# Optimization experiments

Hardware: AMD Instinct MI355X
Metric: run time of the kernel (lower is better)

## Reference

```python
import jax, jax.numpy as jnp
import numpy as np

N = 50000
E = 800000
F_IN = 128
H1, C1 = 8, 32   # conv1: heads=8, out_channels=32 -> concat 256
H2, C2 = 1, 32   # conv2: heads=1, out_channels=32
NEG_SLOPE = 0.2


def setup_inputs() -> dict:
    key = jax.random.key(0)
    ks = jax.random.split(key, 10)
    x = jax.random.normal(ks[0], (N, F_IN), dtype=jnp.float32)
    edge_index = jax.random.randint(ks[1], (2, E), 0, N, dtype=jnp.int64)
    s1 = 1.0 / np.sqrt(F_IN)
    s2 = 1.0 / np.sqrt(H1 * C1)
    return {
        "x": x,
        "edge_index": edge_index,
        "W1": jax.random.normal(ks[2], (F_IN, H1 * C1), dtype=jnp.float32) * s1,
        "b1": jnp.zeros((H1 * C1,), dtype=jnp.float32),
        "att_src1": jax.random.normal(ks[3], (1, H1, C1), dtype=jnp.float32) * s1,
        "att_dst1": jax.random.normal(ks[4], (1, H1, C1), dtype=jnp.float32) * s1,
        "W2": jax.random.normal(ks[5], (H1 * C1, H2 * C2), dtype=jnp.float32) * s2,
        "b2": jnp.zeros((H2 * C2,), dtype=jnp.float32),
        "att_src2": jax.random.normal(ks[6], (1, H2, C2), dtype=jnp.float32) * s2,
        "att_dst2": jax.random.normal(ks[7], (1, H2, C2), dtype=jnp.float32) * s2,
    }


def _gat_conv(x, src, tgt, W, b, att_src, att_dst, heads, ch):
    n = x.shape[0]
    h = (x @ W).reshape(n, heads, ch)                      # [N,H,C]
    a_s = jnp.sum(h * att_src, axis=-1)                    # [N,H]
    a_d = jnp.sum(h * att_dst, axis=-1)                    # [N,H]
    e = jax.nn.leaky_relu(a_s[src] + a_d[tgt], NEG_SLOPE)  # [E',H]
    m = jax.ops.segment_max(e, tgt, num_segments=n)        # per-target max
    e = jnp.exp(e - m[tgt])
    denom = jax.ops.segment_sum(e, tgt, num_segments=n)
    alpha = e / denom[tgt]                                 # edge softmax over in-edges
    msg = h[src] * alpha[:, :, None]                       # [E',H,C]
    out = jax.ops.segment_sum(msg, tgt, num_segments=n)    # scatter-add at targets
    return out.reshape(n, heads * ch) + b


def reference(x, edge_index, W1, b1, att_src1, att_dst1, W2, b2, att_src2, att_dst2):
    n = x.shape[0]
    # PyG GATConv adds self-loops inside each conv; same augmented edge set both layers.
    loops = jnp.arange(n, dtype=edge_index.dtype)
    src = jnp.concatenate([edge_index[0], loops])  # message source j
    tgt = jnp.concatenate([edge_index[1], loops])  # message target i
    h = _gat_conv(x, src, tgt, W1, b1, att_src1, att_dst1, H1, C1)
    h = jax.nn.elu(h)
    h = _gat_conv(h, src, tgt, W2, b2, att_src2, att_dst2, H2, C2)
    return jax.nn.elu(h)
```

## Files before the change

kernel.cpp:

```cpp
#include <hip/hip_runtime.h>
#include <hip/hip_fp16.h>
#include <cmath>

#define NNODES 50000
#define NEDGES 800000
#define ETOT   (NEDGES + NNODES)
#define FIN    128
#define NH1    8
#define NC1    32
#define HC1    256
#define NC2    32

#define NBUCK  ((NNODES + 63) / 64)
#define BCAP   1536
#define EPB    4096

using half8 = __attribute__((ext_vector_type(8))) _Float16;
using f32x4 = __attribute__((ext_vector_type(4))) float;

__device__ __forceinline__ float lrelu(float x) { return x > 0.f ? x : 0.2f * x; }

#define NB_W1    ((FIN * HC1 + 255) / 256)
#define NB_W2    ((HC1 * NC2 + 255) / 256)
#define NB_P1    ((ETOT + EPB - 1) / EPB)

__global__ void __launch_bounds__(256) prep_k(const float* __restrict__ W1,
        __half* __restrict__ W1t, const float* __restrict__ W2, __half* __restrict__ W2t,
        const int* __restrict__ ei, int* __restrict__ bcnt, unsigned* __restrict__ pairs) {
    __shared__ int lcnt[NBUCK];
    __shared__ int gbase[NBUCK];
    int b = blockIdx.x;
    if (b < NB_W1) {
        int i = b * 256 + threadIdx.x;
        if (i < FIN * HC1) {
            int k = i / HC1, n = i - k * HC1;
            W1t[(size_t)n * FIN + k] = __float2half(W1[i]);
        }
        return;
    }
    b -= NB_W1;
    if (b < NB_W2) {
        int i = b * 256 + threadIdx.x;
        if (i < HC1 * NC2) {
            int k = i / NC2, n = i - k * NC2;
            W2t[(size_t)n * HC1 + k] = __float2half(W2[i]);
        }
        return;
    }
    b -= NB_W2;
    for (int i = threadIdx.x; i < NBUCK; i += 256) lcnt[i] = 0;
    __syncthreads();
    int e0 = b * EPB + threadIdx.x;
    int bk[16]; int rk[16]; unsigned pk[16];
#pragma unroll
    for (int k = 0; k < 16; ++k) {
        int e = e0 + k * 256;
        bk[k] = -1;
        if (e < ETOT) {
            int s, t;
            if (e < NEDGES) { s = ei[e]; t = ei[NEDGES + e]; } else { s = t = e - NEDGES; }
            int bb = t >> 6;
            bk[k] = bb;
            rk[k] = atomicAdd(&lcnt[bb], 1);
            pk[k] = ((unsigned)(t & 63) << 16) | (unsigned)s;
        }
    }
    __syncthreads();
    for (int i = threadIdx.x; i < NBUCK; i += 256) {
        int c = lcnt[i];
        gbase[i] = c ? atomicAdd(bcnt + i, c) : 0;
    }
    __syncthreads();
#pragma unroll
    for (int k = 0; k < 16; ++k) {
        if (bk[k] >= 0) {
            int pos = gbase[bk[k]] + rk[k];
            if (pos < BCAP) pairs[(size_t)bk[k] * BCAP + pos] = pk[k];
        }
    }
}

__global__ void __launch_bounds__(256) combo_k(const unsigned* __restrict__ pairs,
        const int* __restrict__ bcnt, int* __restrict__ csr,
        int* __restrict__ rp_start, int* __restrict__ cntT,
        const float* __restrict__ x, const __half* __restrict__ Bt,
        const float* __restrict__ att_s, const float* __restrict__ att_d,
        __half* __restrict__ C, float* __restrict__ as_, float* __restrict__ ad_) {
    __shared__ int lcnt64[64];
    __shared__ int base64[64];
    __shared__ unsigned short binned[BCAP];
    if (blockIdx.x < NBUCK) {
        int b = blockIdx.x;
        int nb = bcnt[b]; nb = nb < BCAP ? nb : BCAP;
        if (threadIdx.x < 64) lcnt64[threadIdx.x] = 0;
        __syncthreads();
        unsigned ps[6]; int rks[6]; bool vld[6];
#pragma unroll
        for (int k = 0; k < 6; ++k) {
            int i = threadIdx.x + k * 256;
            vld[k] = i < nb;
            if (vld[k]) {
                unsigned p = pairs[(size_t)b * BCAP + i];
                ps[k] = p;
                rks[k] = atomicAdd(&lcnt64[p >> 16], 1);
            }
        }
        __syncthreads();
        if (threadIdx.x < 64) {
            int v = lcnt64[threadIdx.x];
            int inc = v;
#pragma unroll
            for (int ofs = 1; ofs < 64; ofs <<= 1) {
                int o = __shfl_up(inc, ofs, 64);
                if ((int)threadIdx.x >= ofs) inc += o;
            }
            base64[threadIdx.x] = inc - v;
        }
        __syncthreads();
#pragma unroll
        for (int k = 0; k < 6; ++k) {
            if (vld[k]) binned[base64[ps[k] >> 16] + rks[k]] = (unsigned short)(ps[k] & 0xFFFFu);
        }
        __syncthreads();
        for (int i = threadIdx.x; i < nb; i += 256)
            csr[(size_t)b * BCAP + i] = binned[i];
        if (threadIdx.x < 64) {
            int t = b * 64 + threadIdx.x;
            if (t < NNODES) {
                rp_start[t] = b * BCAP + base64[threadIdx.x];
                cntT[t] = lcnt64[threadIdx.x];
            }
        }
        return;
    }
    const _Float16* Bf = (const _Float16*)Bt;
    int blk = blockIdx.x - NBUCK;
    int wv = threadIdx.x >> 6, lane = threadIdx.x & 63;
    int r16 = lane & 15, kg = lane >> 4;
    int bm = blk * 16;
    int arow = bm + r16; if (arow >= NNODES) arow = NNODES - 1;
    f32x4 acc[4] = {};
#pragma unroll
    for (int kt = 0; kt < FIN; kt += 32) {
        const float4* xr = (const float4*)(x + (size_t)arow * FIN + kt + kg * 8);
        float4 f0 = xr[0], f1 = xr[1];
        half8 a;
        a[0] = (_Float16)f0.x; a[1] = (_Float16)f0.y; a[2] = (_Float16)f0.z; a[3] = (_Float16)f0.w;
        a[4] = (_Float16)f1.x; a[5] = (_Float16)f1.y; a[6] = (_Float16)f1.z; a[7] = (_Float16)f1.w;
#pragma unroll
        for (int ct = 0; ct < 4; ++ct) {
            int col = wv * 64 + ct * 16 + r16;
            half8 bfr = *(const half8*)(Bf + (size_t)col * FIN + kt + kg * 8);
            acc[ct] = __builtin_amdgcn_mfma_f32_16x16x32_f16(a, bfr, acc[ct], 0, 0, 0);
        }
    }
#pragma unroll
    for (int ct = 0; ct < 4; ++ct)
#pragma unroll
        for (int r = 0; r < 4; ++r) {
            int orow = bm + kg * 4 + r;
            if (orow < NNODES)
                C[(size_t)orow * HC1 + wv * 64 + ct * 16 + r16] = __float2half(acc[ct][r]);
        }
#pragma unroll
    for (int P = 0; P < 2; ++P) {
        int head = 2 * wv + P;
        float ws0 = att_s[head * 32 + r16], ws1 = att_s[head * 32 + 16 + r16];
        float wd0 = att_d[head * 32 + r16], wd1 = att_d[head * 32 + 16 + r16];
        float sv[4], dv[4];
#pragma unroll
        for (int r = 0; r < 4; ++r) {
            sv[r] = acc[2 * P][r] * ws0 + acc[2 * P + 1][r] * ws1;
            dv[r] = acc[2 * P][r] * wd0 + acc[2 * P + 1][r] * wd1;
#pragma unroll
            for (int ofs = 1; ofs < 16; ofs <<= 1) {
                sv[r] += __shfl_xor(sv[r], ofs, 64);
                dv[r] += __shfl_xor(dv[r], ofs, 64);
            }
        }
#pragma unroll
        for (int r = 0; r < 4; ++r) {
            int orow = bm + kg * 4 + r;
            if (r16 == r && orow < NNODES) {
                as_[orow * NH1 + head] = sv[r];
                ad_[orow * NH1 + head] = dv[r];
            }
        }
    }
}

__global__ void __launch_bounds__(256) mgemm2_k(const __half* __restrict__ A,
        const __half* __restrict__ Bt, const float* __restrict__ att_s,
        const float* __restrict__ att_d, __half* __restrict__ C,
        float* __restrict__ as_, float* __restrict__ ad_) {
    const _Float16* Af = (const _Float16*)A;
    const _Float16* Bf = (const _Float16*)Bt;
    int wv = threadIdx.x >> 6, lane = threadIdx.x & 63;
    int r16 = lane & 15, kg = lane >> 4;
    int bm = blockIdx.x * 64 + wv * 16;
    int arow = bm + r16; if (arow >= NNODES) arow = NNODES - 1;
    f32x4 acc[2] = {};
#pragma unroll
    for (int kt = 0; kt < HC1; kt += 32) {
        half8 a = *(const half8*)(Af + (size_t)arow * HC1 + kt + kg * 8);
#pragma unroll
        for (int ct = 0; ct < 2; ++ct) {
            half8 b = *(const half8*)(Bf + (size_t)(ct * 16 + r16) * HC1 + kt + kg * 8);
            acc[ct] = __builtin_amdgcn_mfma_f32_16x16x32_f16(a, b, acc[ct], 0, 0, 0);
        }
    }
#pragma unroll
    for (int ct = 0; ct < 2; ++ct)
#pragma unroll
        for (int r = 0; r < 4; ++r) {
            int orow = bm + kg * 4 + r;
            if (orow < NNODES)
                C[(size_t)orow * NC2 + ct * 16 + r16] = __float2half(acc[ct][r]);
        }
    float ws0 = att_s[r16], ws1 = att_s[16 + r16];
    float wd0 = att_d[r16], wd1 = att_d[16 + r16];
    float sv[4], dv[4];
#pragma unroll
    for (int r = 0; r < 4; ++r) {
        sv[r] = acc[0][r] * ws0 + acc[1][r] * ws1;
        dv[r] = acc[0][r] * wd0 + acc[1][r] * wd1;
#pragma unroll
        for (int ofs = 1; ofs < 16; ofs <<= 1) {
            sv[r] += __shfl_xor(sv[r], ofs, 64);
            dv[r] += __shfl_xor(dv[r], ofs, 64);
        }
    }
#pragma unroll
    for (int r = 0; r < 4; ++r) {
        int orow = bm + kg * 4 + r;
        if (r16 == r && orow < NNODES) { as_[orow] = sv[r]; ad_[orow] = dv[r]; }
    }
}

__global__ void __launch_bounds__(256) gather1_k(const int* __restrict__ rp_start,
        const int* __restrict__ cntT, const int* __restrict__ csr,
        const __half* __restrict__ h, const float* __restrict__ as_,
        const float* __restrict__ ad_, const float* __restrict__ bias,
        __half* __restrict__ out) {
    int t = blockIdx.x * 4 + (threadIdx.x >> 6);
    int lane = threadIdx.x & 63;
    if (t >= NNODES) return;
    int hh = lane & 7;
    int hd = lane >> 3;
    float adv = ad_[t * NH1 + hh];
    int n = cntT[t];
    const int* cb = csr + rp_start[t];
    const uint2* h4 = (const uint2*)h;
    float4 acc = make_float4(0.f, 0.f, 0.f, 0.f);
    float dpart = 0.f;

    int slot = lane >> 3;
    bool val0 = slot < n;
    int sj0 = cb[val0 ? slot : 0];
    float a0 = as_[sj0 * NH1 + hh];

    for (int i = 0; i < n; i += 8) {
        int ii = i + 8 + slot;
        bool val1 = ii < n;
        int sj1 = cb[val1 ? ii : 0];
        float a1 = as_[sj1 * NH1 + hh];
        float p = val0 ? expf(lrelu(a0 + adv)) : 0.f;
        dpart += p;
        uint2 raw[8];
#pragma unroll
        for (int j = 0; j < 8; ++j) {
            int s = __shfl(sj0, 8 * j, 64);
            raw[j] = h4[(size_t)s * 64 + lane];
        }
#pragma unroll
        for (int j = 0; j < 8; ++j) {
            float al = __shfl(p, 8 * j + hd, 64);
            float2 f0 = __half22float2(*(const __half2*)&raw[j].x);
            float2 f1 = __half22float2(*(const __half2*)&raw[j].y);
            acc.x += al * f0.x; acc.y += al * f0.y;
            acc.z += al * f1.x; acc.w += al * f1.y;
        }
        sj0 = sj1; a0 = a1; val0 = val1;
    }
    dpart += __shfl_xor(dpart, 8, 64);
    dpart += __shfl_xor(dpart, 16, 64);
    dpart += __shfl_xor(dpart, 32, 64);
    float inv = __shfl(1.f / dpart, hd, 64);
    float4 bv = ((const float4*)bias)[lane];
    float4 r;
    r.x = acc.x * inv + bv.x; r.y = acc.y * inv + bv.y;
    r.z = acc.z * inv + bv.z; r.w = acc.w * inv + bv.w;
    r.x = r.x > 0.f ? r.x : expm1f(r.x);
    r.y = r.y > 0.f ? r.y : expm1f(r.y);
    r.z = r.z > 0.f ? r.z : expm1f(r.z);
    r.w = r.w > 0.f ? r.w : expm1f(r.w);
    __half2 p0 = __floats2half2_rn(r.x, r.y);
    __half2 p1 = __floats2half2_rn(r.z, r.w);
    uint2 w; w.x = *(unsigned*)&p0; w.y = *(unsigned*)&p1;
    ((uint2*)out)[(size_t)t * 64 + lane] = w;
}

__global__ void __launch_bounds__(256) gather2_k(const int* __restrict__ rp_start,
        const int* __restrict__ cntT, const int* __restrict__ csr,
        const __half* __restrict__ h, const float* __restrict__ as_,
        const float* __restrict__ ad_, const float* __restrict__ bias,
        float* __restrict__ out) {
    int t = blockIdx.x * 4 + (threadIdx.x >> 6);
    int lane = threadIdx.x & 63;
    if (t >= NNODES) return;
    int q = lane >> 3, f = lane & 7;
    float adv = ad_[t];
    int n = cntT[t];
    const int* cb = csr + rp_start[t];
    const uint2* h8 = (const uint2*)h;
    float4 acc = make_float4(0.f, 0.f, 0.f, 0.f);
    float dpart = 0.f;

    bool val0 = q < n;
    int sj0 = cb[val0 ? q : 0];
    float a0 = as_[sj0];

    for (int i = 0; i < n; i += 8) {
        int ii = i + 8 + q;
        bool val1 = ii < n;
        int sj1 = cb[val1 ? ii : 0];
        float a1 = as_[sj1];
        float p = val0 ? expf(lrelu(a0 + adv)) : 0.f;
        dpart += p;
        uint2 raw[8];
#pragma unroll
        for (int j = 0; j < 8; ++j) {
            int sj = __shfl(sj0, 8 * j, 64);
            raw[j] = h8[(size_t)sj * 8 + f];
        }
#pragma unroll
        for (int j = 0; j < 8; ++j) {
            float al = __shfl(p, 8 * j, 64);
            float2 f0 = __half22float2(*(const __half2*)&raw[j].x);
            float2 f1 = __half22float2(*(const __half2*)&raw[j].y);
            acc.x += al * f0.x; acc.y += al * f0.y;
            acc.z += al * f1.x; acc.w += al * f1.y;
        }
        sj0 = sj1; a0 = a1; val0 = val1;
    }
    dpart += __shfl_xor(dpart, 8, 64);
    dpart += __shfl_xor(dpart, 16, 64);
    dpart += __shfl_xor(dpart, 32, 64);
    if (q == 0) {
        float inv = 1.f / dpart;
        float4 bv = ((const float4*)bias)[f];
        float4 r;
        r.x = acc.x * inv + bv.x; r.y = acc.y * inv + bv.y;
        r.z = acc.z * inv + bv.z; r.w = acc.w * inv + bv.w;
        r.x = r.x > 0.f ? r.x : expm1f(r.x);
        r.y = r.y > 0.f ? r.y : expm1f(r.y);
        r.z = r.z > 0.f ? r.z : expm1f(r.z);
        r.w = r.w > 0.f ? r.w : expm1f(r.w);
        ((float4*)out)[(size_t)t * 8 + f] = r;
    }
}

extern "C" void kernel_launch(void* const* d_in, const int* in_sizes, int n_in,
                              void* d_out, int out_size, void* d_ws, size_t ws_size,
                              hipStream_t stream) {
    const float* x    = (const float*)d_in[0];
    const int*   ei   = (const int*)d_in[1];
    const float* W1   = (const float*)d_in[2];
    const float* b1   = (const float*)d_in[3];
    const float* as1w = (const float*)d_in[4];
    const float* ad1w = (const float*)d_in[5];
    const float* W2   = (const float*)d_in[6];
    const float* b2   = (const float*)d_in[7];
    const float* as2w = (const float*)d_in[8];
    const float* ad2w = (const float*)d_in[9];
    float* out = (float*)d_out;

    float* ws = (float*)d_ws;
    size_t off = 0;
    __half* h1h  = (__half*)(ws + off); off += (size_t)NNODES * HC1 / 2;
    __half* out1h= (__half*)(ws + off); off += (size_t)NNODES * HC1 / 2;
    __half* h2h  = (__half*)(ws + off); off += (size_t)NNODES * NC2 / 2;
    __half* W1t  = (__half*)(ws + off); off += (size_t)FIN * HC1 / 2;
    __half* W2t  = (__half*)(ws + off); off += (size_t)HC1 * NC2 / 2;
    float* as1  = ws + off; off += (size_t)NNODES * NH1;
    float* ad1  = ws + off; off += (size_t)NNODES * NH1;
    float* as2  = ws + off; off += NNODES;
    float* ad2  = ws + off; off += NNODES;
    unsigned* pairs = (unsigned*)(ws + off); off += (size_t)NBUCK * BCAP;
    int* csr      = (int*)(ws + off); off += (size_t)NBUCK * BCAP;
    int* bcnt     = (int*)(ws + off); off += NBUCK;
    int* rp_start = (int*)(ws + off); off += NNODES;
    int* cntT     = (int*)(ws + off); off += NNODES;

    hipMemsetAsync(bcnt, 0, (size_t)NBUCK * 4, stream);
    prep_k<<<NB_W1 + NB_W2 + NB_P1, 256, 0, stream>>>(W1, W1t, W2, W2t, ei, bcnt, pairs);
    combo_k<<<NBUCK + (NNODES + 15) / 16, 256, 0, stream>>>(
        pairs, bcnt, csr, rp_start, cntT, x, W1t, as1w, ad1w, h1h, as1, ad1);

    gather1_k<<<(NNODES + 3) / 4, 256, 0, stream>>>(rp_start, cntT, csr, h1h, as1, ad1, b1, out1h);

    mgemm2_k<<<(NNODES + 63) / 64, 256, 0, stream>>>(out1h, W2t, as2w, ad2w, h2h, as2, ad2);
    gather2_k<<<(NNODES + 3) / 4, 256, 0, stream>>>(rp_start, cntT, csr, h2h, as2, ad2, b2, out);
}
```

Baseline: 198.2 us.

## Fuse layer-2 GEMM into gather1 and move layer-1 GEMM into prep kernel

The layer-2 projection (256->32) and its attention logits are now computed inside gather1 straight from the per-node output held in shared memory. This removes the out1h round trip through global memory and drops the separate mgemm2 kernel. The layer-1 MFMA GEMM moves into the first kernel alongside edge bucketing and reads W1 directly as strided fp32 instead of a pre-transposed fp16 copy, so it no longer waits on the CSR finalisation. The trade-offs are uncoalesced scalar W1 loads in the GEMM and a scalar per-wave dot product in gather1 in place of MFMA.

```diff
diff --git a/kernel.cpp b/kernel.cpp
--- a/kernel.cpp
+++ b/kernel.cpp
@@ -20,220 +20,167 @@
 
 __device__ __forceinline__ float lrelu(float x) { return x > 0.f ? x : 0.2f * x; }
 
-#define NB_W1    ((FIN * HC1 + 255) / 256)
-#define NB_W2    ((HC1 * NC2 + 255) / 256)
-#define NB_P1    ((ETOT + EPB - 1) / EPB)
-
-__global__ void __launch_bounds__(256) prep_k(const float* __restrict__ W1,
-        __half* __restrict__ W1t, const float* __restrict__ W2, __half* __restrict__ W2t,
+#define NB_MG1 ((NNODES + 15) / 16)
+#define NB_P1  ((ETOT + EPB - 1) / EPB)
+#define NB_W2  ((HC1 * NC2 + 255) / 256)
+
+__global__ void __launch_bounds__(256) fused1_k(const float* __restrict__ x,
+        const float* __restrict__ W1, const float* __restrict__ att_s,
+        const float* __restrict__ att_d, __half* __restrict__ C,
+        float* __restrict__ as_, float* __restrict__ ad_,
+        const float* __restrict__ W2, __half* __restrict__ W2t,
         const int* __restrict__ ei, int* __restrict__ bcnt, unsigned* __restrict__ pairs) {
     __shared__ int lcnt[NBUCK];
     __shared__ int gbase[NBUCK];
     int b = blockIdx.x;
-    if (b < NB_W1) {
-        int i = b * 256 + threadIdx.x;
-        if (i < FIN * HC1) {
-            int k = i / HC1, n = i - k * HC1;
-            W1t[(size_t)n * FIN + k] = __float2half(W1[i]);
+    if (b < NB_MG1) {
+        int wv = threadIdx.x >> 6, lane = threadIdx.x & 63;
+        int r16 = lane & 15, kg = lane >> 4;
+        int bm = b * 16;
+        int arow = bm + r16; if (arow >= NNODES) arow = NNODES - 1;
+        f32x4 acc[4] = {};
+#pragma unroll
+        for (int kt = 0; kt < FIN; kt += 32) {
+            const float4* xr = (const float4*)(x + (size_t)arow * FIN + kt + kg * 8);
+            float4 f0 = xr[0], f1 = xr[1];
+            half8 a;
+            a[0] = (_Float16)f0.x; a[1] = (_Float16)f0.y; a[2] = (_Float16)f0.z; a[3] = (_Float16)f0.w;
+            a[4] = (_Float16)f1.x; a[5] = (_Float16)f1.y; a[6] = (_Float16)f1.z; a[7] = (_Float16)f1.w;
+#pragma unroll
+            for (int ct = 0; ct < 4; ++ct) {
+                int col = wv * 64 + ct * 16 + r16;
+                half8 bf;
+#pragma unroll
+                for (int j = 0; j < 8; ++j)
+                    bf[j] = (_Float16)W1[(size_t)(kt + kg * 8 + j) * HC1 + col];
+                acc[ct] = __builtin_amdgcn_mfma_f32_16x16x32_f16(a, bf, acc[ct], 0, 0, 0);
+            }
+        }
+#pragma unroll
+        for (int ct = 0; ct < 4; ++ct)
+#pragma unroll
+            for (int r = 0; r < 4; ++r) {
+                int orow = bm + kg * 4 + r;
+                if (orow < NNODES)
+                    C[(size_t)orow * HC1 + wv * 64 + ct * 16 + r16] = __float2half(acc[ct][r]);
+            }
+#pragma unroll
+        for (int P = 0; P < 2; ++P) {
+            int head = 2 * wv + P;
+            float ws0 = att_s[head * 32 + r16], ws1 = att_s[head * 32 + 16 + r16];
+            float wd0 = att_d[head * 32 + r16], wd1 = att_d[head * 32 + 16 + r16];
+            float sv[4], dv[4];
+#pragma unroll
+            for (int r = 0; r < 4; ++r) {
+                sv[r] = acc[2 * P][r] * ws0 + acc[2 * P + 1][r] * ws1;
+                dv[r] = acc[2 * P][r] * wd0 + acc[2 * P + 1][r] * wd1;
+#pragma unroll
+                for (int ofs = 1; ofs < 16; ofs <<= 1) {
+                    sv[r] += __shfl_xor(sv[r], ofs, 64);
+                    dv[r] += __shfl_xor(dv[r], ofs, 64);
+                }
+            }
+#pragma unroll
+            for (int r = 0; r < 4; ++r) {
+                int orow = bm + kg * 4 + r;
+                if (r16 == r && orow < NNODES) {
+                    as_[orow * NH1 + head] = sv[r];
+                    ad_[orow * NH1 + head] = dv[r];
+                }
+            }
         }
         return;
     }
-    b -= NB_W1;
-    if (b < NB_W2) {
+    b -= NB_MG1;
+    if (b < NB_P1) {
+        for (int i = threadIdx.x; i < NBUCK; i += 256) lcnt[i] = 0;
+        __syncthreads();
+        int e0 = b * EPB + threadIdx.x;
+        int bk[16]; int rk[16]; unsigned pk[16];
+#pragma unroll
+        for (int k = 0; k < 16; ++k) {
+            int e = e0 + k * 256;
+            bk[k] = -1;
+            if (e < ETOT) {
+                int s, t;
+                if (e < NEDGES) { s = ei[e]; t = ei[NEDGES + e]; } else { s = t = e - NEDGES; }
+                int bb = t >> 6;
+                bk[k] = bb;
+                rk[k] = atomicAdd(&lcnt[bb], 1);
+                pk[k] = ((unsigned)(t & 63) << 16) | (unsigned)s;
+            }
+        }
+        __syncthreads();
+        for (int i = threadIdx.x; i < NBUCK; i += 256) {
+            int c = lcnt[i];
+            gbase[i] = c ? atomicAdd(bcnt + i, c) : 0;
+        }
+        __syncthreads();
+#pragma unroll
+        for (int k = 0; k < 16; ++k) {
+            if (bk[k] >= 0) {
+                int pos = gbase[bk[k]] + rk[k];
+                if (pos < BCAP) pairs[(size_t)bk[k] * BCAP + pos] = pk[k];
+            }
+        }
+        return;
+    }
+    b -= NB_P1;
+    {
         int i = b * 256 + threadIdx.x;
         if (i < HC1 * NC2) {
             int k = i / NC2, n = i - k * NC2;
             W2t[(size_t)n * HC1 + k] = __float2half(W2[i]);
         }
-        return;
-    }
-    b -= NB_W2;
-    for (int i = threadIdx.x; i < NBUCK; i += 256) lcnt[i] = 0;
-    __syncthreads();
-    int e0 = b * EPB + threadIdx.x;
-    int bk[16]; int rk[16]; unsigned pk[16];
-#pragma unroll
-    for (int k = 0; k < 16; ++k) {
-        int e = e0 + k * 256;
-        bk[k] = -1;
-        if (e < ETOT) {
-            int s, t;
-            if (e < NEDGES) { s = ei[e]; t = ei[NEDGES + e]; } else { s = t = e - NEDGES; }
-            int bb = t >> 6;
-            bk[k] = bb;
-            rk[k] = atomicAdd(&lcnt[bb], 1);
-            pk[k] = ((unsigned)(t & 63) << 16) | (unsigned)s;
-        }
-    }
-    __syncthreads();
-    for (int i = threadIdx.x; i < NBUCK; i += 256) {
-        int c = lcnt[i];
-        gbase[i] = c ? atomicAdd(bcnt + i, c) : 0;
-    }
-    __syncthreads();
-#pragma unroll
-    for (int k = 0; k < 16; ++k) {
-        if (bk[k] >= 0) {
-            int pos = gbase[bk[k]] + rk[k];
-            if (pos < BCAP) pairs[(size_t)bk[k] * BCAP + pos] = pk[k];
-        }
-    }
-}
-
-__global__ void __launch_bounds__(256) combo_k(const unsigned* __restrict__ pairs,
+    }
+}
+
+__global__ void __launch_bounds__(256) pass2_k(const unsigned* __restrict__ pairs,
         const int* __restrict__ bcnt, int* __restrict__ csr,
-        int* __restrict__ rp_start, int* __restrict__ cntT,
-        const float* __restrict__ x, const __half* __restrict__ Bt,
-        const float* __restrict__ att_s, const float* __restrict__ att_d,
-        __half* __restrict__ C, float* __restrict__ as_, float* __restrict__ ad_) {
+        int* __restrict__ rp_start, int* __restrict__ cntT) {
+    int b = blockIdx.x;
+    int nb = bcnt[b]; nb = nb < BCAP ? nb : BCAP;
     __shared__ int lcnt64[64];
     __shared__ int base64[64];
     __shared__ unsigned short binned[BCAP];
-    if (blockIdx.x < NBUCK) {
-        int b = blockIdx.x;
-        int nb = bcnt[b]; nb = nb < BCAP ? nb : BCAP;
-        if (threadIdx.x < 64) lcnt64[threadIdx.x] = 0;
-        __syncthreads();
-        unsigned ps[6]; int rks[6]; bool vld[6];
-#pragma unroll
-        for (int k = 0; k < 6; ++k) {
-            int i = threadIdx.x + k * 256;
-            vld[k] = i < nb;
-            if (vld[k]) {
-                unsigned p = pairs[(size_t)b * BCAP + i];
-                ps[k] = p;
-                rks[k] = atomicAdd(&lcnt64[p >> 16], 1);
-            }
-        }
-        __syncthreads();
-        if (threadIdx.x < 64) {
-            int v = lcnt64[threadIdx.x];
-            int inc = v;
-#pragma unroll
-            for (int ofs = 1; ofs < 64; ofs <<= 1) {
-                int o = __shfl_up(inc, ofs, 64);
-                if ((int)threadIdx.x >= ofs) inc += o;
-            }
-            base64[threadIdx.x] = inc - v;
-        }
-        __syncthreads();
-#pragma unroll
-        for (int k = 0; k < 6; ++k) {
-            if (vld[k]) binned[base64[ps[k] >> 16] + rks[k]] = (unsigned short)(ps[k] & 0xFFFFu);
-        }
-        __syncthreads();
-        for (int i = threadIdx.x; i < nb; i += 256)
-            csr[(size_t)b * BCAP + i] = binned[i];
-        if (threadIdx.x < 64) {
-            int t = b * 64 + threadIdx.x;
-            if (t < NNODES) {
-                rp_start[t] = b * BCAP + base64[threadIdx.x];
-                cntT[t] = lcnt64[threadIdx.x];
-            }
-        }
-        return;
-    }
-    const _Float16* Bf = (const _Float16*)Bt;
-    int blk = blockIdx.x - NBUCK;
-    int wv = threadIdx.x >> 6, lane = threadIdx.x & 63;
-    int r16 = lane & 15, kg = lane >> 4;
-    int bm = blk * 16;
-    int arow = bm + r16; if (arow >= NNODES) arow = NNODES - 1;
-    f32x4 acc[4] = {};
-#pragma unroll
-    for (int kt = 0; kt < FIN; kt += 32) {
-        const float4* xr = (const float4*)(x + (size_t)arow * FIN + kt + kg * 8);
-        float4 f0 = xr[0], f1 = xr[1];
-        half8 a;
-        a[0] = (_Float16)f0.x; a[1] = (_Float16)f0.y; a[2] = (_Float16)f0.z; a[3] = (_Float16)f0.w;
-        a[4] = (_Float16)f1.x; a[5] = (_Float16)f1.y; a[6] = (_Float16)f1.z; a[7] = (_Float16)f1.w;
-#pragma unroll
-        for (int ct = 0; ct < 4; ++ct) {
-            int col = wv * 64 + ct * 16 + r16;
-            half8 bfr = *(const half8*)(Bf + (size_t)col * FIN + kt + kg * 8);
-            acc[ct] = __builtin_amdgcn_mfma_f32_16x16x32_f16(a, bfr, acc[ct], 0, 0, 0);
-        }
-    }
-#pragma unroll
-    for (int ct = 0; ct < 4; ++ct)
-#pragma unroll
-        for (int r = 0; r < 4; ++r) {
-            int orow = bm + kg * 4 + r;
-            if (orow < NNODES)
-                C[(size_t)orow * HC1 + wv * 64 + ct * 16 + r16] = __float2half(acc[ct][r]);
-        }
-#pragma unroll
-    for (int P = 0; P < 2; ++P) {
-        int head = 2 * wv + P;
-        float ws0 = att_s[head * 32 + r16], ws1 = att_s[head * 32 + 16 + r16];
-        float wd0 = att_d[head * 32 + r16], wd1 = att_d[head * 32 + 16 + r16];
-        float sv[4], dv[4];
-#pragma unroll
-        for (int r = 0; r < 4; ++r) {
-            sv[r] = acc[2 * P][r] * ws0 + acc[2 * P + 1][r] * ws1;
-            dv[r] = acc[2 * P][r] * wd0 + acc[2 * P + 1][r] * wd1;
-#pragma unroll
-            for (int ofs = 1; ofs < 16; ofs <<= 1) {
-                sv[r] += __shfl_xor(sv[r], ofs, 64);
-                dv[r] += __shfl_xor(dv[r], ofs, 64);
-            }
-        }
-#pragma unroll
-        for (int r = 0; r < 4; ++r) {
-            int orow = bm + kg * 4 + r;
-            if (r16 == r && orow < NNODES) {
-                as_[orow * NH1 + head] = sv[r];
-                ad_[orow * NH1 + head] = dv[r];
-            }
-        }
-    }
-}
-
-__global__ void __launch_bounds__(256) mgemm2_k(const __half* __restrict__ A,
-        const __half* __restrict__ Bt, const float* __restrict__ att_s,
-        const float* __restrict__ att_d, __half* __restrict__ C,
-        float* __restrict__ as_, float* __restrict__ ad_) {
-    const _Float16* Af = (const _Float16*)A;
-    const _Float16* Bf = (const _Float16*)Bt;
-    int wv = threadIdx.x >> 6, lane = threadIdx.x & 63;
-    int r16 = lane & 15, kg = lane >> 4;
-    int bm = blockIdx.x * 64 + wv * 16;
-    int arow = bm + r16; if (arow >= NNODES) arow = NNODES - 1;
-    f32x4 acc[2] = {};
-#pragma unroll
-    for (int kt = 0; kt < HC1; kt += 32) {
-        half8 a = *(const half8*)(Af + (size_t)arow * HC1 + kt + kg * 8);
-#pragma unroll
-        for (int ct = 0; ct < 2; ++ct) {
-            half8 b = *(const half8*)(Bf + (size_t)(ct * 16 + r16) * HC1 + kt + kg * 8);
-            acc[ct] = __builtin_amdgcn_mfma_f32_16x16x32_f16(a, b, acc[ct], 0, 0, 0);
-        }
-    }
-#pragma unroll
-    for (int ct = 0; ct < 2; ++ct)
-#pragma unroll
-        for (int r = 0; r < 4; ++r) {
-            int orow = bm + kg * 4 + r;
-            if (orow < NNODES)
-                C[(size_t)orow * NC2 + ct * 16 + r16] = __float2half(acc[ct][r]);
-        }
-    float ws0 = att_s[r16], ws1 = att_s[16 + r16];
-    float wd0 = att_d[r16], wd1 = att_d[16 + r16];
-    float sv[4], dv[4];
-#pragma unroll
-    for (int r = 0; r < 4; ++r) {
-        sv[r] = acc[0][r] * ws0 + acc[1][r] * ws1;
-        dv[r] = acc[0][r] * wd0 + acc[1][r] * wd1;
-#pragma unroll
-        for (int ofs = 1; ofs < 16; ofs <<= 1) {
-            sv[r] += __shfl_xor(sv[r], ofs, 64);
-            dv[r] += __shfl_xor(dv[r], ofs, 64);
-        }
-    }
-#pragma unroll
-    for (int r = 0; r < 4; ++r) {
-        int orow = bm + kg * 4 + r;
-        if (r16 == r && orow < NNODES) { as_[orow] = sv[r]; ad_[orow] = dv[r]; }
+    if (threadIdx.x < 64) lcnt64[threadIdx.x] = 0;
+    __syncthreads();
+    unsigned ps[6]; int rks[6]; bool vld[6];
+#pragma unroll
+    for (int k = 0; k < 6; ++k) {
+        int i = threadIdx.x + k * 256;
+        vld[k] = i < nb;
+        if (vld[k]) {
+            unsigned p = pairs[(size_t)b * BCAP + i];
+            ps[k] = p;
+            rks[k] = atomicAdd(&lcnt64[p >> 16], 1);
+        }
+    }
+    __syncthreads();
+    if (threadIdx.x < 64) {
+        int v = lcnt64[threadIdx.x];
+        int inc = v;
+#pragma unroll
+        for (int ofs = 1; ofs < 64; ofs <<= 1) {
+            int o = __shfl_up(inc, ofs, 64);
+            if ((int)threadIdx.x >= ofs) inc += o;
+        }
+        base64[threadIdx.x] = inc - v;
+    }
+    __syncthreads();
+#pragma unroll
+    for (int k = 0; k < 6; ++k) {
+        if (vld[k]) binned[base64[ps[k] >> 16] + rks[k]] = (unsigned short)(ps[k] & 0xFFFFu);
+    }
+    __syncthreads();
+    for (int i = threadIdx.x; i < nb; i += 256)
+        csr[(size_t)b * BCAP + i] = binned[i];
+    if (threadIdx.x < 64) {
+        int t = b * 64 + threadIdx.x;
+        if (t < NNODES) {
+            rp_start[t] = b * BCAP + base64[threadIdx.x];
+            cntT[t] = lcnt64[threadIdx.x];
+        }
     }
 }
 
@@ -241,10 +188,13 @@
         const int* __restrict__ cntT, const int* __restrict__ csr,
         const __half* __restrict__ h, const float* __restrict__ as_,
         const float* __restrict__ ad_, const float* __restrict__ bias,
-        __half* __restrict__ out) {
-    int t = blockIdx.x * 4 + (threadIdx.x >> 6);
+        const __half* __restrict__ W2t, const float* __restrict__ att_s2,
+        const float* __restrict__ att_d2, __half* __restrict__ h2h,
+        float* __restrict__ as2, float* __restrict__ ad2) {
+    __shared__ __half s_o1[4][HC1 + 8];
+    int wg = threadIdx.x >> 6;
+    int t = blockIdx.x * 4 + wg;
     int lane = threadIdx.x & 63;
-    if (t >= NNODES) return;
     int hh = lane & 7;
     int hd = lane >> 3;
     float adv = ad_[t * NH1 + hh];
@@ -296,8 +246,28 @@
     r.w = r.w > 0.f ? r.w : expm1f(r.w);
     __half2 p0 = __floats2half2_rn(r.x, r.y);
     __half2 p1 = __floats2half2_rn(r.z, r.w);
-    uint2 w; w.x = *(unsigned*)&p0; w.y = *(unsigned*)&p1;
-    ((uint2*)out)[(size_t)t * 64 + lane] = w;
+    *(__half2*)&s_o1[wg][4 * lane]     = p0;
+    *(__half2*)&s_o1[wg][4 * lane + 2] = p1;
+    int c = lane & 31, khalf = (lane >> 5) * (HC1 / 2);
+    const __half2* wrow = (const __half2*)(W2t + (size_t)c * HC1 + khalf);
+    const __half2* orow = (const __half2*)&s_o1[wg][khalf];
+    float accd = 0.f;
+#pragma unroll
+    for (int k = 0; k < HC1 / 4; ++k) {
+        float2 av = __half22float2(orow[k]);
+        float2 bw = __half22float2(wrow[k]);
+        accd += av.x * bw.x + av.y * bw.y;
+    }
+    accd += __shfl_xor(accd, 32, 64);
+    if (lane < 32) h2h[(size_t)t * NC2 + c] = __float2half(accd);
+    float sv = accd * att_s2[c];
+    float dv = accd * att_d2[c];
+#pragma unroll
+    for (int ofs = 1; ofs < 32; ofs <<= 1) {
+        sv += __shfl_xor(sv, ofs, 64);
+        dv += __shfl_xor(dv, ofs, 64);
+    }
+    if (lane == 0) { as2[t] = sv; ad2[t] = dv; }
 }
 
 __global__ void __launch_bounds__(256) gather2_k(const int* __restrict__ rp_start,
@@ -378,9 +348,7 @@
     float* ws = (float*)d_ws;
     size_t off = 0;
     __half* h1h  = (__half*)(ws + off); off += (size_t)NNODES * HC1 / 2;
-    __half* out1h= (__half*)(ws + off); off += (size_t)NNODES * HC1 / 2;
     __half* h2h  = (__half*)(ws + off); off += (size_t)NNODES * NC2 / 2;
-    __half* W1t  = (__half*)(ws + off); off += (size_t)FIN * HC1 / 2;
     __half* W2t  = (__half*)(ws + off); off += (size_t)HC1 * NC2 / 2;
     float* as1  = ws + off; off += (size_t)NNODES * NH1;
     float* ad1  = ws + off; off += (size_t)NNODES * NH1;
@@ -393,12 +361,11 @@
     int* cntT     = (int*)(ws + off); off += NNODES;
 
     hipMemsetAsync(bcnt, 0, (size_t)NBUCK * 4, stream);
-    prep_k<<<NB_W1 + NB_W2 + NB_P1, 256, 0, stream>>>(W1, W1t, W2, W2t, ei, bcnt, pairs);
-    combo_k<<<NBUCK + (NNODES + 15) / 16, 256, 0, stream>>>(
-        pairs, bcnt, csr, rp_start, cntT, x, W1t, as1w, ad1w, h1h, as1, ad1);
-
-    gather1_k<<<(NNODES + 3) / 4, 256, 0, stream>>>(rp_start, cntT, csr, h1h, as1, ad1, b1, out1h);
-
-    mgemm2_k<<<(NNODES + 63) / 64, 256, 0, stream>>>(out1h, W2t, as2w, ad2w, h2h, as2, ad2);
-    gather2_k<<<(NNODES + 3) / 4, 256, 0, stream>>>(rp_start, cntT, csr, h2h, as2, ad2, b2, out);
-}
+    fused1_k<<<NB_MG1 + NB_P1 + NB_W2, 256, 0, stream>>>(
+        x, W1, as1w, ad1w, h1h, as1, ad1, W2, W2t, ei, bcnt, pairs);
+    pass2_k<<<NBUCK, 256, 0, stream>>>(pairs, bcnt, csr, rp_start, cntT);
+
+    gather1_k<<<NNODES / 4, 256, 0, stream>>>(rp_start, cntT, csr, h1h, as1, ad1, b1,
+                                              W2t, as2w, ad2w, h2h, as2, ad2);
+    gather2_k<<<NNODES / 4, 256, 0, stream>>>(rp_start, cntT, csr, h2h, as2, ad2, b2, out);
+}
```

Result: slower. 230.7 us (+16.4%).

## Move layer-1 GEMM into the edge-binning kernel, read W1 directly

Applied to the files above, without the earlier changes.

The first GEMM (x·W1 with attention logits) moves from the CSR-finalize kernel into the same launch as edge bucketing and the W2 transpose. The separate fp16 transpose of W1 is dropped, and the GEMM now loads W1 columns with strided scalar fp32 reads and converts them in registers. The CSR finalize pass becomes its own small kernel. The aim is to overlap GEMM work with the first binning pass and remove one dependency on the weight prep, at the cost of uncoalesced, repeated W1 loads in every GEMM block.

```diff
diff --git a/kernel.cpp b/kernel.cpp
--- a/kernel.cpp
+++ b/kernel.cpp
@@ -20,220 +20,167 @@
 
 __device__ __forceinline__ float lrelu(float x) { return x > 0.f ? x : 0.2f * x; }
 
-#define NB_W1    ((FIN * HC1 + 255) / 256)
-#define NB_W2    ((HC1 * NC2 + 255) / 256)
-#define NB_P1    ((ETOT + EPB - 1) / EPB)
-
-__global__ void __launch_bounds__(256) prep_k(const float* __restrict__ W1,
-        __half* __restrict__ W1t, const float* __restrict__ W2, __half* __restrict__ W2t,
+#define NB_MG1 ((NNODES + 15) / 16)
+#define NB_P1  ((ETOT + EPB - 1) / EPB)
+#define NB_W2  ((HC1 * NC2 + 255) / 256)
+
+__global__ void __launch_bounds__(256) fused1_k(const float* __restrict__ x,
+        const float* __restrict__ W1, const float* __restrict__ att_s,
+        const float* __restrict__ att_d, __half* __restrict__ C,
+        float* __restrict__ as_, float* __restrict__ ad_,
+        const float* __restrict__ W2, __half* __restrict__ W2t,
         const int* __restrict__ ei, int* __restrict__ bcnt, unsigned* __restrict__ pairs) {
     __shared__ int lcnt[NBUCK];
     __shared__ int gbase[NBUCK];
     int b = blockIdx.x;
-    if (b < NB_W1) {
-        int i = b * 256 + threadIdx.x;
-        if (i < FIN * HC1) {
-            int k = i / HC1, n = i - k * HC1;
-            W1t[(size_t)n * FIN + k] = __float2half(W1[i]);
+    if (b < NB_MG1) {
+        int wv = threadIdx.x >> 6, lane = threadIdx.x & 63;
+        int r16 = lane & 15, kg = lane >> 4;
+        int bm = b * 16;
+        int arow = bm + r16; if (arow >= NNODES) arow = NNODES - 1;
+        f32x4 acc[4] = {};
+#pragma unroll
+        for (int kt = 0; kt < FIN; kt += 32) {
+            const float4* xr = (const float4*)(x + (size_t)arow * FIN + kt + kg * 8);
+            float4 f0 = xr[0], f1 = xr[1];
+            half8 a;
+            a[0] = (_Float16)f0.x; a[1] = (_Float16)f0.y; a[2] = (_Float16)f0.z; a[3] = (_Float16)f0.w;
+            a[4] = (_Float16)f1.x; a[5] = (_Float16)f1.y; a[6] = (_Float16)f1.z; a[7] = (_Float16)f1.w;
+#pragma unroll
+            for (int ct = 0; ct < 4; ++ct) {
+                int col = wv * 64 + ct * 16 + r16;
+                half8 bf;
+#pragma unroll
+                for (int j = 0; j < 8; ++j)
+                    bf[j] = (_Float16)W1[(size_t)(kt + kg * 8 + j) * HC1 + col];
+                acc[ct] = __builtin_amdgcn_mfma_f32_16x16x32_f16(a, bf, acc[ct], 0, 0, 0);
+            }
+        }
+#pragma unroll
+        for (int ct = 0; ct < 4; ++ct)
+#pragma unroll
+            for (int r = 0; r < 4; ++r) {
+                int orow = bm + kg * 4 + r;
+                if (orow < NNODES)
+                    C[(size_t)orow * HC1 + wv * 64 + ct * 16 + r16] = __float2half(acc[ct][r]);
+            }
+#pragma unroll
+        for (int P = 0; P < 2; ++P) {
+            int head = 2 * wv + P;
+            float ws0 = att_s[head * 32 + r16], ws1 = att_s[head * 32 + 16 + r16];
+            float wd0 = att_d[head * 32 + r16], wd1 = att_d[head * 32 + 16 + r16];
+            float sv[4], dv[4];
+#pragma unroll
+            for (int r = 0; r < 4; ++r) {
+                sv[r] = acc[2 * P][r] * ws0 + acc[2 * P + 1][r] * ws1;
+                dv[r] = acc[2 * P][r] * wd0 + acc[2 * P + 1][r] * wd1;
+#pragma unroll
+                for (int ofs = 1; ofs < 16; ofs <<= 1) {
+                    sv[r] += __shfl_xor(sv[r], ofs, 64);
+                    dv[r] += __shfl_xor(dv[r], ofs, 64);
+                }
+            }
+#pragma unroll
+            for (int r = 0; r < 4; ++r) {
+                int orow = bm + kg * 4 + r;
+                if (r16 == r && orow < NNODES) {
+                    as_[orow * NH1 + head] = sv[r];
+                    ad_[orow * NH1 + head] = dv[r];
+                }
+            }
         }
         return;
     }
-    b -= NB_W1;
-    if (b < NB_W2) {
+    b -= NB_MG1;
+    if (b < NB_P1) {
+        for (int i = threadIdx.x; i < NBUCK; i += 256) lcnt[i] = 0;
+        __syncthreads();
+        int e0 = b * EPB + threadIdx.x;
+        int bk[16]; int rk[16]; unsigned pk[16];
+#pragma unroll
+        for (int k = 0; k < 16; ++k) {
+            int e = e0 + k * 256;
+            bk[k] = -1;
+            if (e < ETOT) {
+                int s, t;
+                if (e < NEDGES) { s = ei[e]; t = ei[NEDGES + e]; } else { s = t = e - NEDGES; }
+                int bb = t >> 6;
+                bk[k] = bb;
+                rk[k] = atomicAdd(&lcnt[bb], 1);
+                pk[k] = ((unsigned)(t & 63) << 16) | (unsigned)s;
+            }
+        }
+        __syncthreads();
+        for (int i = threadIdx.x; i < NBUCK; i += 256) {
+            int c = lcnt[i];
+            gbase[i] = c ? atomicAdd(bcnt + i, c) : 0;
+        }
+        __syncthreads();
+#pragma unroll
+        for (int k = 0; k < 16; ++k) {
+            if (bk[k] >= 0) {
+                int pos = gbase[bk[k]] + rk[k];
+                if (pos < BCAP) pairs[(size_t)bk[k] * BCAP + pos] = pk[k];
+            }
+        }
+        return;
+    }
+    b -= NB_P1;
+    {
         int i = b * 256 + threadIdx.x;
         if (i < HC1 * NC2) {
             int k = i / NC2, n = i - k * NC2;
             W2t[(size_t)n * HC1 + k] = __float2half(W2[i]);
         }
-        return;
-    }
-    b -= NB_W2;
-    for (int i = threadIdx.x; i < NBUCK; i += 256) lcnt[i] = 0;
-    __syncthreads();
-    int e0 = b * EPB + threadIdx.x;
-    int bk[16]; int rk[16]; unsigned pk[16];
-#pragma unroll
-    for (int k = 0; k < 16; ++k) {
-        int e = e0 + k * 256;
-        bk[k] = -1;
-        if (e < ETOT) {
-            int s, t;
-            if (e < NEDGES) { s = ei[e]; t = ei[NEDGES + e]; } else { s = t = e - NEDGES; }
-            int bb = t >> 6;
-            bk[k] = bb;
-            rk[k] = atomicAdd(&lcnt[bb], 1);
-            pk[k] = ((unsigned)(t & 63) << 16) | (unsigned)s;
-        }
-    }
-    __syncthreads();
-    for (int i = threadIdx.x; i < NBUCK; i += 256) {
-        int c = lcnt[i];
-        gbase[i] = c ? atomicAdd(bcnt + i, c) : 0;
-    }
-    __syncthreads();
-#pragma unroll
-    for (int k = 0; k < 16; ++k) {
-        if (bk[k] >= 0) {
-            int pos = gbase[bk[k]] + rk[k];
-            if (pos < BCAP) pairs[(size_t)bk[k] * BCAP + pos] = pk[k];
-        }
-    }
-}
-
-__global__ void __launch_bounds__(256) combo_k(const unsigned* __restrict__ pairs,
+    }
+}
+
+__global__ void __launch_bounds__(256) pass2_k(const unsigned* __restrict__ pairs,
         const int* __restrict__ bcnt, int* __restrict__ csr,
-        int* __restrict__ rp_start, int* __restrict__ cntT,
-        const float* __restrict__ x, const __half* __restrict__ Bt,
-        const float* __restrict__ att_s, const float* __restrict__ att_d,
-        __half* __restrict__ C, float* __restrict__ as_, float* __restrict__ ad_) {
+        int* __restrict__ rp_start, int* __restrict__ cntT) {
+    int b = blockIdx.x;
+    int nb = bcnt[b]; nb = nb < BCAP ? nb : BCAP;
     __shared__ int lcnt64[64];
     __shared__ int base64[64];
     __shared__ unsigned short binned[BCAP];
-    if (blockIdx.x < NBUCK) {
-        int b = blockIdx.x;
-        int nb = bcnt[b]; nb = nb < BCAP ? nb : BCAP;
-        if (threadIdx.x < 64) lcnt64[threadIdx.x] = 0;
-        __syncthreads();
-        unsigned ps[6]; int rks[6]; bool vld[6];
-#pragma unroll
-        for (int k = 0; k < 6; ++k) {
-            int i = threadIdx.x + k * 256;
-            vld[k] = i < nb;
-            if (vld[k]) {
-                unsigned p = pairs[(size_t)b * BCAP + i];
-                ps[k] = p;
-                rks[k] = atomicAdd(&lcnt64[p >> 16], 1);
-            }
-        }
-        __syncthreads();
-        if (threadIdx.x < 64) {
-            int v = lcnt64[threadIdx.x];
-            int inc = v;
-#pragma unroll
-            for (int ofs = 1; ofs < 64; ofs <<= 1) {
-                int o = __shfl_up(inc, ofs, 64);
-                if ((int)threadIdx.x >= ofs) inc += o;
-            }
-            base64[threadIdx.x] = inc - v;
-        }
-        __syncthreads();
-#pragma unroll
-        for (int k = 0; k < 6; ++k) {
-            if (vld[k]) binned[base64[ps[k] >> 16] + rks[k]] = (unsigned short)(ps[k] & 0xFFFFu);
-        }
-        __syncthreads();
-        for (int i = threadIdx.x; i < nb; i += 256)
-            csr[(size_t)b * BCAP + i] = binned[i];
-        if (threadIdx.x < 64) {
-            int t = b * 64 + threadIdx.x;
-            if (t < NNODES) {
-                rp_start[t] = b * BCAP + base64[threadIdx.x];
-                cntT[t] = lcnt64[threadIdx.x];
-            }
-        }
-        return;
-    }
-    const _Float16* Bf = (const _Float16*)Bt;
-    int blk = blockIdx.x - NBUCK;
-    int wv = threadIdx.x >> 6, lane = threadIdx.x & 63;
-    int r16 = lane & 15, kg = lane >> 4;
-    int bm = blk * 16;
-    int arow = bm + r16; if (arow >= NNODES) arow = NNODES - 1;
-    f32x4 acc[4] = {};
-#pragma unroll
-    for (int kt = 0; kt < FIN; kt += 32) {
-        const float4* xr = (const float4*)(x + (size_t)arow * FIN + kt + kg * 8);
-        float4 f0 = xr[0], f1 = xr[1];
-        half8 a;
-        a[0] = (_Float16)f0.x; a[1] = (_Float16)f0.y; a[2] = (_Float16)f0.z; a[3] = (_Float16)f0.w;
-        a[4] = (_Float16)f1.x; a[5] = (_Float16)f1.y; a[6] = (_Float16)f1.z; a[7] = (_Float16)f1.w;
-#pragma unroll
-        for (int ct = 0; ct < 4; ++ct) {
-            int col = wv * 64 + ct * 16 + r16;
-            half8 bfr = *(const half8*)(Bf + (size_t)col * FIN + kt + kg * 8);
-            acc[ct] = __builtin_amdgcn_mfma_f32_16x16x32_f16(a, bfr, acc[ct], 0, 0, 0);
-        }
-    }
-#pragma unroll
-    for (int ct = 0; ct < 4; ++ct)
-#pragma unroll
-        for (int r = 0; r < 4; ++r) {
-            int orow = bm + kg * 4 + r;
-            if (orow < NNODES)
-                C[(size_t)orow * HC1 + wv * 64 + ct * 16 + r16] = __float2half(acc[ct][r]);
-        }
-#pragma unroll
-    for (int P = 0; P < 2; ++P) {
-        int head = 2 * wv + P;
-        float ws0 = att_s[head * 32 + r16], ws1 = att_s[head * 32 + 16 + r16];
-        float wd0 = att_d[head * 32 + r16], wd1 = att_d[head * 32 + 16 + r16];
-        float sv[4], dv[4];
-#pragma unroll
-        for (int r = 0; r < 4; ++r) {
-            sv[r] = acc[2 * P][r] * ws0 + acc[2 * P + 1][r] * ws1;
-            dv[r] = acc[2 * P][r] * wd0 + acc[2 * P + 1][r] * wd1;
-#pragma unroll
-            for (int ofs = 1; ofs < 16; ofs <<= 1) {
-                sv[r] += __shfl_xor(sv[r], ofs, 64);
-                dv[r] += __shfl_xor(dv[r], ofs, 64);
-            }
-        }
-#pragma unroll
-        for (int r = 0; r < 4; ++r) {
-            int orow = bm + kg * 4 + r;
-            if (r16 == r && orow < NNODES) {
-                as_[orow * NH1 + head] = sv[r];
-                ad_[orow * NH1 + head] = dv[r];
-            }
-        }
-    }
-}
-
-__global__ void __launch_bounds__(256) mgemm2_k(const __half* __restrict__ A,
-        const __half* __restrict__ Bt, const float* __restrict__ att_s,
-        const float* __restrict__ att_d, __half* __restrict__ C,
-        float* __restrict__ as_, float* __restrict__ ad_) {
-    const _Float16* Af = (const _Float16*)A;
-    const _Float16* Bf = (const _Float16*)Bt;
-    int wv = threadIdx.x >> 6, lane = threadIdx.x & 63;
-    int r16 = lane & 15, kg = lane >> 4;
-    int bm = blockIdx.x * 64 + wv * 16;
-    int arow = bm + r16; if (arow >= NNODES) arow = NNODES - 1;
-    f32x4 acc[2] = {};
-#pragma unroll
-    for (int kt = 0; kt < HC1; kt += 32) {
-        half8 a = *(const half8*)(Af + (size_t)arow * HC1 + kt + kg * 8);
-#pragma unroll
-        for (int ct = 0; ct < 2; ++ct) {
-            half8 b = *(const half8*)(Bf + (size_t)(ct * 16 + r16) * HC1 + kt + kg * 8);
-            acc[ct] = __builtin_amdgcn_mfma_f32_16x16x32_f16(a, b, acc[ct], 0, 0, 0);
-        }
-    }
-#pragma unroll
-    for (int ct = 0; ct < 2; ++ct)
-#pragma unroll
-        for (int r = 0; r < 4; ++r) {
-            int orow = bm + kg * 4 + r;
-            if (orow < NNODES)
-                C[(size_t)orow * NC2 + ct * 16 + r16] = __float2half(acc[ct][r]);
-        }
-    float ws0 = att_s[r16], ws1 = att_s[16 + r16];
-    float wd0 = att_d[r16], wd1 = att_d[16 + r16];
-    float sv[4], dv[4];
-#pragma unroll
-    for (int r = 0; r < 4; ++r) {
-        sv[r] = acc[0][r] * ws0 + acc[1][r] * ws1;
-        dv[r] = acc[0][r] * wd0 + acc[1][r] * wd1;
-#pragma unroll
-        for (int ofs = 1; ofs < 16; ofs <<= 1) {
-            sv[r] += __shfl_xor(sv[r], ofs, 64);
-            dv[r] += __shfl_xor(dv[r], ofs, 64);
-        }
-    }
-#pragma unroll
-    for (int r = 0; r < 4; ++r) {
-        int orow = bm + kg * 4 + r;
-        if (r16 == r && orow < NNODES) { as_[orow] = sv[r]; ad_[orow] = dv[r]; }
+    if (threadIdx.x < 64) lcnt64[threadIdx.x] = 0;
+    __syncthreads();
+    unsigned ps[6]; int rks[6]; bool vld[6];
+#pragma unroll
+    for (int k = 0; k < 6; ++k) {
+        int i = threadIdx.x + k * 256;
+        vld[k] = i < nb;
+        if (vld[k]) {
+            unsigned p = pairs[(size_t)b * BCAP + i];
+            ps[k] = p;
+            rks[k] = atomicAdd(&lcnt64[p >> 16], 1);
+        }
+    }
+    __syncthreads();
+    if (threadIdx.x < 64) {
+        int v = lcnt64[threadIdx.x];
+        int inc = v;
+#pragma unroll
+        for (int ofs = 1; ofs < 64; ofs <<= 1) {
+            int o = __shfl_up(inc, ofs, 64);
+            if ((int)threadIdx.x >= ofs) inc += o;
+        }
+        base64[threadIdx.x] = inc - v;
+    }
+    __syncthreads();
+#pragma unroll
+    for (int k = 0; k < 6; ++k) {
+        if (vld[k]) binned[base64[ps[k] >> 16] + rks[k]] = (unsigned short)(ps[k] & 0xFFFFu);
+    }
+    __syncthreads();
+    for (int i = threadIdx.x; i < nb; i += 256)
+        csr[(size_t)b * BCAP + i] = binned[i];
+    if (threadIdx.x < 64) {
+        int t = b * 64 + threadIdx.x;
+        if (t < NNODES) {
+            rp_start[t] = b * BCAP + base64[threadIdx.x];
+            cntT[t] = lcnt64[threadIdx.x];
+        }
     }
 }
 
@@ -300,6 +247,54 @@
     ((uint2*)out)[(size_t)t * 64 + lane] = w;
 }
 
+__global__ void __launch_bounds__(256) mgemm2_k(const __half* __restrict__ A,
+        const __half* __restrict__ Bt, const float* __restrict__ att_s,
+        const float* __restrict__ att_d, __half* __restrict__ C,
+        float* __restrict__ as_, float* __restrict__ ad_) {
+    const _Float16* Af = (const _Float16*)A;
+    const _Float16* Bf = (const _Float16*)Bt;
+    int wv = threadIdx.x >> 6, lane = threadIdx.x & 63;
+    int r16 = lane & 15, kg = lane >> 4;
+    int bm = blockIdx.x * 64 + wv * 16;
+    int arow = bm + r16; if (arow >= NNODES) arow = NNODES - 1;
+    f32x4 acc[2] = {};
+#pragma unroll
+    for (int kt = 0; kt < HC1; kt += 32) {
+        half8 a = *(const half8*)(Af + (size_t)arow * HC1 + kt + kg * 8);
+#pragma unroll
+        for (int ct = 0; ct < 2; ++ct) {
+            half8 b = *(const half8*)(Bf + (size_t)(ct * 16 + r16) * HC1 + kt + kg * 8);
+            acc[ct] = __builtin_amdgcn_mfma_f32_16x16x32_f16(a, b, acc[ct], 0, 0, 0);
+        }
+    }
+#pragma unroll
+    for (int ct = 0; ct < 2; ++ct)
+#pragma unroll
+        for (int r = 0; r < 4; ++r) {
+            int orow = bm + kg * 4 + r;
+            if (orow < NNODES)
+                C[(size_t)orow * NC2 + ct * 16 + r16] = __float2half(acc[ct][r]);
+        }
+    float ws0 = att_s[r16], ws1 = att_s[16 + r16];
+    float wd0 = att_d[r16], wd1 = att_d[16 + r16];
+    float sv[4], dv[4];
+#pragma unroll
+    for (int r = 0; r < 4; ++r) {
+        sv[r] = acc[0][r] * ws0 + acc[1][r] * ws1;
+        dv[r] = acc[0][r] * wd0 + acc[1][r] * wd1;
+#pragma unroll
+        for (int ofs = 1; ofs < 16; ofs <<= 1) {
+            sv[r] += __shfl_xor(sv[r], ofs, 64);
+            dv[r] += __shfl_xor(dv[r], ofs, 64);
+        }
+    }
+#pragma unroll
+    for (int r = 0; r < 4; ++r) {
+        int orow = bm + kg * 4 + r;
+        if (r16 == r && orow < NNODES) { as_[orow] = sv[r]; ad_[orow] = dv[r]; }
+    }
+}
+
 __global__ void __launch_bounds__(256) gather2_k(const int* __restrict__ rp_start,
         const int* __restrict__ cntT, const int* __restrict__ csr,
         const __half* __restrict__ h, const float* __restrict__ as_,
@@ -380,7 +375,6 @@
     __half* h1h  = (__half*)(ws + off); off += (size_t)NNODES * HC1 / 2;
     __half* out1h= (__half*)(ws + off); off += (size_t)NNODES * HC1 / 2;
     __half* h2h  = (__half*)(ws + off); off += (size_t)NNODES * NC2 / 2;
-    __half* W1t  = (__half*)(ws + off); off += (size_t)FIN * HC1 / 2;
     __half* W2t  = (__half*)(ws + off); off += (size_t)HC1 * NC2 / 2;
     float* as1  = ws + off; off += (size_t)NNODES * NH1;
     float* ad1  = ws + off; off += (size_t)NNODES * NH1;
@@ -393,12 +387,11 @@
     int* cntT     = (int*)(ws + off); off += NNODES;
 
     hipMemsetAsync(bcnt, 0, (size_t)NBUCK * 4, stream);
-    prep_k<<<NB_W1 + NB_W2 + NB_P1, 256, 0, stream>>>(W1, W1t, W2, W2t, ei, bcnt, pairs);
-    combo_k<<<NBUCK + (NNODES + 15) / 16, 256, 0, stream>>>(
-        pairs, bcnt, csr, rp_start, cntT, x, W1t, as1w, ad1w, h1h, as1, ad1);
-
-    gather1_k<<<(NNODES + 3) / 4, 256, 0, stream>>>(rp_start, cntT, csr, h1h, as1, ad1, b1, out1h);
-
+    fused1_k<<<NB_MG1 + NB_P1 + NB_W2, 256, 0, stream>>>(
+        x, W1, as1w, ad1w, h1h, as1, ad1, W2, W2t, ei, bcnt, pairs);
+    pass2_k<<<NBUCK, 256, 0, stream>>>(pairs, bcnt, csr, rp_start, cntT);
+
+    gather1_k<<<NNODES / 4, 256, 0, stream>>>(rp_start, cntT, csr, h1h, as1, ad1, b1, out1h);
     mgemm2_k<<<(NNODES + 63) / 64, 256, 0, stream>>>(out1h, W2t, as2w, ad2w, h2h, as2, ad2);
-    gather2_k<<<(NNODES + 3) / 4, 256, 0, stream>>>(rp_start, cntT, csr, h2h, as2, ad2, b2, out);
-}
+    gather2_k<<<NNODES / 4, 256, 0, stream>>>(rp_start, cntT, csr, h2h, as2, ad2, b2, out);
+}
```

After: 185.8 us (median of 2 runs). 1.07x faster.
